# Optimization experiments

Measured on AMD Instinct MI355X. Metric: run time of the kernel, lower is better.

Reference implementation:

```python
import jax, jax.numpy as jnp
import numpy as np

WEIGHT_LOC = 1.0
WEIGHT_FEAT = 1.0
TOP_K = 16  # feat_vector[:16].mean() in the original
EPS = 1e-12  # F.normalize default eps


def _l2_normalize(x, axis):
    return x / jnp.maximum(jnp.linalg.norm(x, axis=axis, keepdims=True), EPS)


def _pair_sim(gfa, cda, gfb, cdb):
    # gfa, gfb: (N, F) already row-normalized; cda, cdb: (N, 2)
    n = gfa.shape[0]
    # diagonal of gfa @ gfb.T (trace/gate in the original is computed but unused)
    v = jnp.sum(gfa * gfb, axis=-1)              # (N,)
    vs = -jnp.sort(-v)                            # sort descending
    sim_feat = jnp.mean(vs[:TOP_K])
    w = vs - jnp.min(vs)
    weight = (w[:, None] * w[None, :]).reshape(-1)          # (N*N,) outer product
    weight = weight / jnp.maximum(jnp.linalg.norm(weight), EPS)
    da = cda[:, None, :] - cda[None, :, :]        # (N, N, 2)
    db = cdb[:, None, :] - cdb[None, :, :]        # (N, N, 2)
    loc_dis = jnp.sum((da - db) ** 2, axis=-1).reshape(-1)  # (N*N,)
    dis_loc = jnp.mean(loc_dis * weight)
    return WEIGHT_FEAT * sim_feat - WEIGHT_LOC * dis_loc


def setup_inputs() -> dict:
    key = jax.random.key(0)
    k1, k2, k3, k4 = jax.random.split(key, 4)
    R, N, F = 8, 1024, 256
    return {
        "graph_feat_a": jax.random.normal(k1, (R, N, F), dtype=jnp.float32),
        "coord_a": jax.random.uniform(k2, (R, N, 2), dtype=jnp.float32),
        "graph_feat_b": jax.random.normal(k3, (R, N, F), dtype=jnp.float32),
        "coord_b": jax.random.uniform(k4, (R, N, 2), dtype=jnp.float32),
    }


def reference(graph_feat_a, coord_a, graph_feat_b, coord_b):
    gfa = _l2_normalize(graph_feat_a, axis=-1)  # F.normalize(gf, dim=1) on (N,F)
    gfb = _l2_normalize(graph_feat_b, axis=-1)
    # vectorize the original double Python loop over (N_rot_a, N_rot_b) pairs
    inner = jax.vmap(_pair_sim, in_axes=(None, None, 0, 0))
    outer = jax.vmap(inner, in_axes=(0, 0, None, None))
    sims = outer(gfa, coord_a, gfb, coord_b)    # (R, R)
    return jnp.max(sims)
```

## Files before the change

### kernel.cpp

```cpp
#include <hip/hip_runtime.h>
#include <math.h>

#define EPS 1e-12f

constexpr int N = 1024;
constexpr int F = 256;
constexpr int NPAIR = 64;

template <int CTRL>
__device__ __forceinline__ float dppAdd(float x) {
    int y = __builtin_amdgcn_update_dpp(0, __float_as_int(x), CTRL, 0xf, 0xf, true);
    return x + __int_as_float(y);
}
__device__ __forceinline__ float waveSum64(float x) {
    x = dppAdd<0x111>(x);
    x = dppAdd<0x112>(x);
    x = dppAdd<0x114>(x);
    x = dppAdd<0x118>(x);
    x = dppAdd<0x142>(x);
    x = dppAdd<0x143>(x);
    return x;
}

__device__ __forceinline__ float dot4(float4 a, float4 b) {
    return a.x * b.x + a.y * b.y + a.z * b.z + a.w * b.w;
}

__device__ inline void atomicMaxFloat(float* addr, float val) {
    unsigned int* ua = (unsigned int*)addr;
    unsigned int old = __hip_atomic_load(ua, __ATOMIC_RELAXED, __HIP_MEMORY_SCOPE_AGENT);
    while (__uint_as_float(old) < val) {
        unsigned int assumed = old;
        old = atomicCAS(ua, assumed, __float_as_uint(val));
        if (old == assumed) break;
    }
}

__global__ __launch_bounds__(1024) void dot_kernel(const float* __restrict__ gfa,
                                                   const float* __restrict__ gfb,
                                                   float* __restrict__ v,
                                                   float* __restrict__ out) {
    __shared__ float4 rows[4][16][64];
    const unsigned b    = blockIdx.x;
    const unsigned tid  = threadIdx.x;
    const unsigned sub  = tid >> 8;
    const unsigned t    = tid & 255;
    const unsigned lane = tid & 63;
    const unsigned wv   = t >> 6;
    const unsigned n    = b * 4 + sub;

    if (b == 0 && tid == 0)
        __hip_atomic_store(out, -INFINITY, __ATOMIC_RELAXED, __HIP_MEMORY_SCOPE_AGENT);

    #pragma unroll
    for (int rep = 0; rep < 4; ++rep) {
        const int idx = rep * 256 + (int)t;
        const int row = idx >> 6;
        const int c4  = idx & 63;
        const float* src = (row < 8) ? gfa + ((size_t)row * N + n) * F
                                     : gfb + ((size_t)(row - 8) * N + n) * F;
        rows[sub][row][c4] = ((const float4*)src)[c4];
    }
    __syncthreads();

    const int ra0 = 2 * (int)wv, ra1 = ra0 + 1;
    const float4 a0 = rows[sub][ra0][lane];
    const float4 a1 = rows[sub][ra1][lane];
    float4 bb[8];
    #pragma unroll
    for (int rb = 0; rb < 8; ++rb) bb[rb] = rows[sub][8 + rb][lane];

    float na0 = waveSum64(dot4(a0, a0));
    float na1 = waveSum64(dot4(a1, a1));
    float nb[8], d0[8], d1[8];
    #pragma unroll
    for (int rb = 0; rb < 8; ++rb) {
        nb[rb] = waveSum64(dot4(bb[rb], bb[rb]));
        d0[rb] = waveSum64(dot4(a0, bb[rb]));
        d1[rb] = waveSum64(dot4(a1, bb[rb]));
    }
    if (lane == 63) {
        const float ia0 = 1.f / fmaxf(sqrtf(na0), EPS);
        const float ia1 = 1.f / fmaxf(sqrtf(na1), EPS);
        #pragma unroll
        for (int rb = 0; rb < 8; ++rb) {
            const float ib = 1.f / fmaxf(sqrtf(nb[rb]), EPS);
            v[(size_t)(ra0 * 8 + rb) * N + n] = d0[rb] * ia0 * ib;
            v[(size_t)(ra1 * 8 + rb) * N + n] = d1[rb] * ia1 * ib;
        }
    }
}

__global__ __launch_bounds__(256) void pair_kernel(const float* __restrict__ v,
                                                   const float* __restrict__ ca,
                                                   const float* __restrict__ cb,
                                                   float* __restrict__ out) {
    const int p = blockIdx.x;
    const int ra = p >> 3, rb = p & 7;
    const int tid = threadIdx.x;
    const int lane = tid & 63, wv = tid >> 6;
    __shared__ float s[N];
    __shared__ float rbuf[4][6];

    const float4* pa4 = (const float4*)(ca + (size_t)ra * N * 2) + tid * 2;
    const float4* pb4 = (const float4*)(cb + (size_t)rb * N * 2) + tid * 2;
    const float4 a01 = pa4[0], a23 = pa4[1];
    const float4 b01 = pb4[0], b23 = pb4[1];

    const float4 xv = ((const float4*)(v + (size_t)p * N))[tid];
    float x[4] = { xv.x, xv.y, xv.z, xv.w };

    #pragma unroll
    for (int k = 2; k <= 1024; k <<= 1) {
        #pragma unroll
        for (int j = k >> 1; j >= 1; j >>= 1) {
            if (j >= 256) {
                ((float4*)s)[tid] = make_float4(x[0], x[1], x[2], x[3]);
                __syncthreads();
                const float4 yv = ((const float4*)s)[tid ^ (j >> 2)];
                const float y[4] = { yv.x, yv.y, yv.z, yv.w };
                const bool up = ((tid & (k >> 2)) == 0);
                const bool hi = ((tid & (j >> 2)) != 0);
                const bool keepMin = (hi != up);
                #pragma unroll
                for (int e = 0; e < 4; ++e)
                    x[e] = keepMin ? fminf(x[e], y[e]) : fmaxf(x[e], y[e]);
                __syncthreads();
            } else if (j >= 4) {
                const int J = j >> 2;
                const bool up = ((tid & (k >> 2)) == 0);
                const bool hi = ((lane & J) != 0);
                const bool keepMin = (hi != up);
                #pragma unroll
                for (int e = 0; e < 4; ++e) {
                    const float y = __shfl_xor(x[e], J);
                    x[e] = keepMin ? fminf(x[e], y) : fmaxf(x[e], y);
                }
            } else if (j == 2) {
                #pragma unroll
                for (int e = 0; e < 2; ++e) {
                    const int f = e + 2;
                    const bool up = (((tid * 4 + e) & k) == 0);
                    const float a = x[e], b2 = x[f];
                    x[e] = up ? fminf(a, b2) : fmaxf(a, b2);
                    x[f] = up ? fmaxf(a, b2) : fminf(a, b2);
                }
            } else {
                #pragma unroll
                for (int e = 0; e < 4; e += 2) {
                    const int f = e + 1;
                    const bool up = (((tid * 4 + e) & k) == 0);
                    const float a = x[e], b2 = x[f];
                    x[e] = up ? fminf(a, b2) : fmaxf(a, b2);
                    x[f] = up ? fmaxf(a, b2) : fminf(a, b2);
                }
            }
        }
    }

    ((float4*)s)[tid] = make_float4(x[0], x[1], x[2], x[3]);
    __syncthreads();

    const float vmin = s[0];
    const float4 dsc = ((const float4*)s)[255 - tid];
    const float u[4] = { dsc.w - vmin, dsc.z - vmin, dsc.y - vmin, dsc.x - vmin };

    float t16p = 0.f;
    if (tid < 4) {
        const float4 q = ((const float4*)s)[252 + tid];
        t16p = q.x + q.y + q.z + q.w;
    }

    float Su = 0.f, U2 = 0.f, A = 0.f, Bx = 0.f, By = 0.f;
    {
        const float exs[4] = { a01.x - b01.x, a01.z - b01.z, a23.x - b23.x, a23.z - b23.z };
        const float eys[4] = { a01.y - b01.y, a01.w - b01.w, a23.y - b23.y, a23.w - b23.w };
        #pragma unroll
        for (int e = 0; e < 4; ++e) {
            const float uu = u[e], ex = exs[e], ey = eys[e];
            Su += uu; U2 += uu * uu;
            A  += uu * (ex * ex + ey * ey);
            Bx += uu * ex; By += uu * ey;
        }
    }

    float vals[6] = { Su, U2, A, Bx, By, t16p };
    #pragma unroll
    for (int m = 0; m < 6; ++m) {
        const float r = waveSum64(vals[m]);
        if (lane == 63) rbuf[wv][m] = r;
    }
    __syncthreads();

    if (tid == 0) {
        float acc[6];
        #pragma unroll
        for (int m = 0; m < 6; ++m)
            acc[m] = rbuf[0][m] + rbuf[1][m] + rbuf[2][m] + rbuf[3][m];
        const float sim_feat = acc[5] * (1.f / 16.f);
        const float denom = (float)N * (float)N * fmaxf(acc[1], EPS);
        const float dis_loc = (2.f * acc[0] * acc[2] - 2.f * (acc[3] * acc[3] + acc[4] * acc[4])) / denom;
        atomicMaxFloat(out, sim_feat - dis_loc);
    }
}

extern "C" void kernel_launch(void* const* d_in, const int* in_sizes, int n_in,
                              void* d_out, int out_size, void* d_ws, size_t ws_size,
                              hipStream_t stream) {
    const float* gfa = (const float*)d_in[0];
    const float* ca  = (const float*)d_in[1];
    const float* gfb = (const float*)d_in[2];
    const float* cb  = (const float*)d_in[3];
    float* out = (float*)d_out;

    float* v = (float*)d_ws;

    dot_kernel<<<256, 1024, 0, stream>>>(gfa, gfb, v, out);
    pair_kernel<<<NPAIR, 256, 0, stream>>>(v, ca, cb, out);
}
```

Before: 19.99 us.

## Compute all 64 rotation-pair dots per row in one wave without LDS

The dot kernel changes from 1024-thread blocks that stage 16 rows in shared memory into 1024 single-wave blocks, one per node index. Each wave loads all 8 a-rows and 8 b-rows straight into registers and computes the norms and all 64 dot products with DPP reductions. This removes the LDS staging, the block barrier and the recomputed norms across waves. In exchange, each wave does serial work for 64+16 reductions, raises register pressure, and has fewer threads in flight to hide the 16 KB of loads per wave.

```diff
diff --git a/kernel.cpp b/kernel.cpp
--- a/kernel.cpp
+++ b/kernel.cpp
@@ -36,57 +36,45 @@
     }
 }
 
-__global__ __launch_bounds__(1024) void dot_kernel(const float* __restrict__ gfa,
-                                                   const float* __restrict__ gfb,
-                                                   float* __restrict__ v,
-                                                   float* __restrict__ out) {
-    __shared__ float4 rows[4][16][64];
-    const unsigned b    = blockIdx.x;
-    const unsigned tid  = threadIdx.x;
-    const unsigned sub  = tid >> 8;
-    const unsigned t    = tid & 255;
-    const unsigned lane = tid & 63;
-    const unsigned wv   = t >> 6;
-    const unsigned n    = b * 4 + sub;
-
-    if (b == 0 && tid == 0)
+__global__ __launch_bounds__(64) void dot_kernel(const float* __restrict__ gfa,
+                                                 const float* __restrict__ gfb,
+                                                 float* __restrict__ v,
+                                                 float* __restrict__ out) {
+    const int n = blockIdx.x;
+    const int lane = threadIdx.x;
+
+    if (n == 0 && lane == 0)
         __hip_atomic_store(out, -INFINITY, __ATOMIC_RELAXED, __HIP_MEMORY_SCOPE_AGENT);
 
-    #pragma unroll
-    for (int rep = 0; rep < 4; ++rep) {
-        const int idx = rep * 256 + (int)t;
-        const int row = idx >> 6;
-        const int c4  = idx & 63;
-        const float* src = (row < 8) ? gfa + ((size_t)row * N + n) * F
-                                     : gfb + ((size_t)(row - 8) * N + n) * F;
-        rows[sub][row][c4] = ((const float4*)src)[c4];
-    }
-    __syncthreads();
-
-    const int ra0 = 2 * (int)wv, ra1 = ra0 + 1;
-    const float4 a0 = rows[sub][ra0][lane];
-    const float4 a1 = rows[sub][ra1][lane];
-    float4 bb[8];
-    #pragma unroll
-    for (int rb = 0; rb < 8; ++rb) bb[rb] = rows[sub][8 + rb][lane];
-
-    float na0 = waveSum64(dot4(a0, a0));
-    float na1 = waveSum64(dot4(a1, a1));
-    float nb[8], d0[8], d1[8];
-    #pragma unroll
-    for (int rb = 0; rb < 8; ++rb) {
-        nb[rb] = waveSum64(dot4(bb[rb], bb[rb]));
-        d0[rb] = waveSum64(dot4(a0, bb[rb]));
-        d1[rb] = waveSum64(dot4(a1, bb[rb]));
-    }
-    if (lane == 63) {
-        const float ia0 = 1.f / fmaxf(sqrtf(na0), EPS);
-        const float ia1 = 1.f / fmaxf(sqrtf(na1), EPS);
-        #pragma unroll
-        for (int rb = 0; rb < 8; ++rb) {
-            const float ib = 1.f / fmaxf(sqrtf(nb[rb]), EPS);
-            v[(size_t)(ra0 * 8 + rb) * N + n] = d0[rb] * ia0 * ib;
-            v[(size_t)(ra1 * 8 + rb) * N + n] = d1[rb] * ia1 * ib;
+    const float4* A4 = (const float4*)gfa;
+    const float4* B4 = (const float4*)gfb;
+
+    float4 a[8], b[8];
+    #pragma unroll
+    for (int r = 0; r < 8; ++r) {
+        a[r] = A4[((size_t)r * N + n) * 64 + lane];
+        b[r] = B4[((size_t)r * N + n) * 64 + lane];
+    }
+
+    float inva[8], invb[8];
+    #pragma unroll
+    for (int r = 0; r < 8; ++r) {
+        const float na = waveSum64(dot4(a[r], a[r]));
+        const float nb = waveSum64(dot4(b[r], b[r]));
+        inva[r] = 1.f / fmaxf(sqrtf(na), EPS);
+        invb[r] = 1.f / fmaxf(sqrtf(nb), EPS);
+    }
+
+    #pragma unroll
+    for (int ra = 0; ra < 8; ++ra) {
+        float d[8];
+        #pragma unroll
+        for (int rb = 0; rb < 8; ++rb)
+            d[rb] = waveSum64(dot4(a[ra], b[rb]));
+        if (lane == 63) {
+            #pragma unroll
+            for (int rb = 0; rb < 8; ++rb)
+                v[(size_t)(ra * 8 + rb) * N + n] = d[rb] * inva[ra] * invb[rb];
         }
     }
 }
@@ -215,6 +203,6 @@
 
     float* v = (float*)d_ws;
 
-    dot_kernel<<<256, 1024, 0, stream>>>(gfa, gfb, v, out);
+    dot_kernel<<<N, 64, 0, stream>>>(gfa, gfb, v, out);
     pair_kernel<<<NPAIR, 256, 0, stream>>>(v, ca, cb, out);
 }
```

Result: faster. 17.69 us (-11.5%).
